# Optimization experiments

Hardware: AMD Instinct MI355X
Metric: run time of the kernel (lower is better)

## Reference

```python
import jax, jax.numpy as jnp
import numpy as np

N_NODES = 50000
N_EDGES = 400000
D = 512
LN_EPS = 1e-5


def setup_inputs() -> dict:
    key = jax.random.key(0)
    k0, k1, k2, k3 = jax.random.split(key, 4)
    x = jax.random.normal(k0, (N_NODES, D), dtype=jnp.float32)
    src = jax.random.randint(k1, (N_EDGES,), 0, N_NODES, dtype=jnp.int64)
    dst = jax.random.randint(k2, (N_EDGES,), 0, N_NODES, dtype=jnp.int64)
    W = jax.random.normal(k3, (D, D), dtype=jnp.float32) * 0.05
    b = jnp.zeros((D,), dtype=jnp.float32)
    gamma = jnp.ones((D,), dtype=jnp.float32)
    beta = jnp.zeros((D,), dtype=jnp.float32)
    return {"x": x, "W": W, "b": b, "gamma": gamma, "beta": beta, "src": src, "dst": dst}


def reference(x, W, b, gamma, beta, src, dst):
    n = x.shape[0]
    ones = jnp.ones(src.shape, dtype=x.dtype)
    # DGL GraphConv norm='both': clamp degrees to >= 1
    deg_out = jnp.clip(jax.ops.segment_sum(ones, src, num_segments=n), 1.0)  # [N]
    deg_in = jnp.clip(jax.ops.segment_sum(ones, dst, num_segments=n), 1.0)   # [N]
    h = x * jax.lax.rsqrt(deg_out)[:, None]                 # [N, D] src normalization
    agg = jax.ops.segment_sum(h[src], dst, num_segments=n)  # gather->scatter-add SpMM
    h = agg * jax.lax.rsqrt(deg_in)[:, None]                # dst normalization
    h = h @ W + b                                           # dense linear
    # LayerNorm over last dim
    mu = jnp.mean(h, axis=-1, keepdims=True)
    var = jnp.mean(jnp.square(h - mu), axis=-1, keepdims=True)
    h = (h - mu) * jax.lax.rsqrt(var + LN_EPS) * gamma + beta
    # torch nn.GELU default = exact erf GELU
    return jax.nn.gelu(h, approximate=False)
```

## Files before the change

### kernel.cpp

```cpp
#include <hip/hip_runtime.h>
#include <hip/hip_bf16.h>

#define D 512

typedef __attribute__((ext_vector_type(8))) short bf16x8;
typedef __attribute__((ext_vector_type(4))) float f32x4;

__device__ inline float b2f(short h) {
    union { unsigned u; float f; } c;
    c.u = ((unsigned)(unsigned short)h) << 16;
    return c.f;
}

__global__ void k_hist(const int* __restrict__ src, const int* __restrict__ dst,
                       int* __restrict__ deg_out, int* __restrict__ deg_in, int E) {
    int e = blockIdx.x * 256 + threadIdx.x;
    if (e < E) {
        atomicAdd(&deg_out[src[e]], 1);
        atomicAdd(&deg_in[dst[e]], 1);
    }
}

__global__ __launch_bounds__(256)
void k_scale(const float* __restrict__ x, const int* __restrict__ deg_out,
             __hip_bfloat16* __restrict__ xs, int total16) {
    int i = blockIdx.x * 256 + threadIdx.x;
    if (i >= total16) return;
    int node = i >> 6;
    float w = rsqrtf((float)max(deg_out[node], 1));
    const float4* p = (const float4*)(x + (size_t)i * 8);
    float4 a = p[0], b = p[1];
    union { float4 f4; __hip_bfloat16 h[8]; } o;
    o.h[0] = __float2bfloat16(a.x * w);
    o.h[1] = __float2bfloat16(a.y * w);
    o.h[2] = __float2bfloat16(a.z * w);
    o.h[3] = __float2bfloat16(a.w * w);
    o.h[4] = __float2bfloat16(b.x * w);
    o.h[5] = __float2bfloat16(b.y * w);
    o.h[6] = __float2bfloat16(b.z * w);
    o.h[7] = __float2bfloat16(b.w * w);
    *(float4*)(xs + (size_t)i * 8) = o.f4;
}

__global__ void k_scan1(const int* __restrict__ deg_in, int* __restrict__ row_start,
                        int* __restrict__ partials, int N) {
    __shared__ int sm[1024];
    int tid = threadIdx.x;
    int i = blockIdx.x * 1024 + tid;
    int v = (i < N) ? deg_in[i] : 0;
    sm[tid] = v;
    __syncthreads();
    int acc = v;
    #pragma unroll
    for (int off = 1; off < 1024; off <<= 1) {
        int t = (tid >= off) ? sm[tid - off] : 0;
        __syncthreads();
        acc += t;
        sm[tid] = acc;
        __syncthreads();
    }
    if (i < N) row_start[i] = acc - v;
    if (tid == 1023) partials[blockIdx.x] = acc;
}

__global__ void k_scan2w(int* __restrict__ partials, int* __restrict__ row_start,
                         int nb, int N) {
    int lane = threadIdx.x;
    int orig = (lane < nb) ? partials[lane] : 0;
    int v = orig;
    #pragma unroll
    for (int off = 1; off < 64; off <<= 1) {
        int t = __shfl_up(v, off, 64);
        if (lane >= off) v += t;
    }
    if (lane < nb) partials[lane] = v - orig;
    if (lane == 63) row_start[N] = v;
}

__global__ void k_scan2s(int* __restrict__ partials, int* __restrict__ row_start,
                         int nb, int N) {
    if (threadIdx.x == 0 && blockIdx.x == 0) {
        int run = 0;
        for (int b = 0; b < nb; b++) { int t = partials[b]; partials[b] = run; run += t; }
        row_start[N] = run;
    }
}

__global__ void k_scan3(int* __restrict__ row_start, const int* __restrict__ partials, int N) {
    int i = blockIdx.x * 256 + threadIdx.x;
    if (i < N) row_start[i] += partials[i >> 10];
}

__global__ void k_fill(const int* __restrict__ src, const int* __restrict__ dst,
                       const int* __restrict__ row_start, int* __restrict__ cursor,
                       int* __restrict__ csr_src, int E) {
    int e = blockIdx.x * 256 + threadIdx.x;
    if (e < E) {
        int d = dst[e];
        int slot = atomicAdd(&cursor[d], 1);
        csr_src[row_start[d] + slot] = src[e];
    }
}

__global__ __launch_bounds__(1024)
void k_spmm(const __hip_bfloat16* __restrict__ xs, const int* __restrict__ row_start,
            const int* __restrict__ csr_src, __hip_bfloat16* __restrict__ Ap, int N) {
    int wid = threadIdx.x >> 6;
    int lane = threadIdx.x & 63;
    int node = blockIdx.x * 16 + wid;
    if (node >= N) return;
    int rs = row_start[node], re = row_start[node + 1];

    float acc[8];
    #pragma unroll
    for (int k = 0; k < 8; k++) acc[k] = 0.f;
    const __hip_bfloat16* xl = xs + (size_t)lane * 8;

    int j = rs;
    for (; j + 4 <= re; j += 4) {
        int s0 = csr_src[j], s1 = csr_src[j + 1], s2 = csr_src[j + 2], s3 = csr_src[j + 3];
        bf16x8 v0 = *(const bf16x8*)(xl + (size_t)s0 * D);
        bf16x8 v1 = *(const bf16x8*)(xl + (size_t)s1 * D);
        bf16x8 v2 = *(const bf16x8*)(xl + (size_t)s2 * D);
        bf16x8 v3 = *(const bf16x8*)(xl + (size_t)s3 * D);
        #pragma unroll
        for (int k = 0; k < 8; k++)
            acc[k] += (b2f(v0[k]) + b2f(v1[k])) + (b2f(v2[k]) + b2f(v3[k]));
    }
    for (; j < re; j++) {
        int s = csr_src[j];
        bf16x8 v = *(const bf16x8*)(xl + (size_t)s * D);
        #pragma unroll
        for (int k = 0; k < 8; k++) acc[k] += b2f(v[k]);
    }

    float rn = rsqrtf((float)max(re - rs, 1));
    union { float4 f4; __hip_bfloat16 h[8]; } o;
    #pragma unroll
    for (int k = 0; k < 8; k++) o.h[k] = __float2bfloat16(acc[k] * rn);
    *(float4*)((char*)Ap + ((size_t)(node >> 4) * 1024 + lane * 16 + (node & 15)) * 16) = o.f4;
}

__global__ __launch_bounds__(256)
void k_spmm_f32(const float* __restrict__ x, const int* __restrict__ row_start,
                const int* __restrict__ csr_src, const int* __restrict__ deg_out,
                __hip_bfloat16* __restrict__ A, int N) {
    int wid = threadIdx.x >> 6;
    int lane = threadIdx.x & 63;
    int node = blockIdx.x * 4 + wid;
    if (node >= N) return;
    int rs = row_start[node], re = row_start[node + 1];
    float4 acc0 = {0.f, 0.f, 0.f, 0.f};
    float4 acc1 = {0.f, 0.f, 0.f, 0.f};
    const float* xl = x + (size_t)lane * 8;
    for (int j = rs; j < re; j++) {
        int s = csr_src[j];
        float w = rsqrtf((float)max(deg_out[s], 1));
        const float4* p = (const float4*)(xl + (size_t)s * D);
        float4 a = p[0], b = p[1];
        acc0.x += a.x * w; acc0.y += a.y * w; acc0.z += a.z * w; acc0.w += a.w * w;
        acc1.x += b.x * w; acc1.y += b.y * w; acc1.z += b.z * w; acc1.w += b.w * w;
    }
    float rn = rsqrtf((float)max(re - rs, 1));
    union { float4 f4; __hip_bfloat16 h[8]; } o;
    o.h[0] = __float2bfloat16(acc0.x * rn);
    o.h[1] = __float2bfloat16(acc0.y * rn);
    o.h[2] = __float2bfloat16(acc0.z * rn);
    o.h[3] = __float2bfloat16(acc0.w * rn);
    o.h[4] = __float2bfloat16(acc1.x * rn);
    o.h[5] = __float2bfloat16(acc1.y * rn);
    o.h[6] = __float2bfloat16(acc1.z * rn);
    o.h[7] = __float2bfloat16(acc1.w * rn);
    *(float4*)(A + (size_t)node * D + lane * 8) = o.f4;
}

__global__ void k_packw2(const float* __restrict__ W, __hip_bfloat16* __restrict__ Wp) {
    int bid = blockIdx.x;
    int c = bid >> 7, kt = (bid >> 3) & 15, ntc = bid & 7;
    int lane = threadIdx.x;
    int k0 = kt * 32 + (lane >> 4) * 8;
    int n  = (c * 8 + ntc) * 16 + (lane & 15);
    union { float4 f4; __hip_bfloat16 h[8]; } o;
    #pragma unroll
    for (int j = 0; j < 8; j++)
        o.h[j] = __float2bfloat16(W[(size_t)(k0 + j) * D + n]);
    *(float4*)(Wp + ((size_t)bid * 64 + lane) * 8) = o.f4;
}

__global__ void k_packw(const float* __restrict__ W, __hip_bfloat16* __restrict__ Wp) {
    int tile = blockIdx.x;
    int lane = threadIdx.x;
    int kt = tile >> 5, nt = tile & 31;
    int k0 = kt * 32 + (lane >> 4) * 8;
    int n  = nt * 16 + (lane & 15);
    union { float4 f4; __hip_bfloat16 h[8]; } o;
    #pragma unroll
    for (int j = 0; j < 8; j++)
        o.h[j] = __float2bfloat16(W[(size_t)(k0 + j) * D + n]);
    *(float4*)(Wp + ((size_t)tile * 64 + lane) * 8) = o.f4;
}

__global__ __launch_bounds__(512, 4)
void k_gemm3(const __hip_bfloat16* __restrict__ Ap, const __hip_bfloat16* __restrict__ Wp,
             const float* __restrict__ bias, const float* __restrict__ gamma,
             const float* __restrict__ beta, float* __restrict__ out, int M) {
    __shared__ float s_sum[64][4];
    __shared__ float s_sq[64][4];

    int tid = threadIdx.x;
    int wid = tid >> 6, lane = tid & 63;
    int wm = wid >> 2, wn = wid & 3;
    int l4 = lane >> 4, coll = lane & 15;
    int tb = blockIdx.x * 64;
    int rgmax = ((M + 15) >> 4) - 1;

    int rg0 = (tb >> 4) + wm * 2;
    int rgA = min(rg0, rgmax);
    int rgB = min(rg0 + 1, rgmax);
    const char* a0 = (const char*)Ap + (size_t)rgA * 16384 + (size_t)lane * 16;
    const char* a1 = (const char*)Ap + (size_t)rgB * 16384 + (size_t)lane * 16;
    const char* wb = (const char*)Wp + ((size_t)(wn * 128) * 64 + lane) * 16;

    f32x4 acc0[8], acc1[8];
    #pragma unroll
    for (int t = 0; t < 8; t++) { acc0[t] = (f32x4){0,0,0,0}; acc1[t] = (f32x4){0,0,0,0}; }

    for (int kt = 0; kt < 16; kt++) {
        bf16x8 af0 = *(const bf16x8*)(a0 + (size_t)kt * 1024);
        bf16x8 af1 = *(const bf16x8*)(a1 + (size_t)kt * 1024);
        const char* wk = wb + (size_t)kt * 8192;
        #pragma unroll
        for (int t = 0; t < 8; t++) {
            bf16x8 bf = *(const bf16x8*)(wk + (size_t)t * 1024);
            acc0[t] = __builtin_amdgcn_mfma_f32_16x16x32_bf16(af0, bf, acc0[t], 0, 0, 0);
            acc1[t] = __builtin_amdgcn_mfma_f32_16x16x32_bf16(af1, bf, acc1[t], 0, 0, 0);
        }
    }

    float bia[8], gam[8], bet[8];
    #pragma unroll
    for (int t = 0; t < 8; t++) {
        int col = wn * 128 + t * 16 + coll;
        bia[t] = bias[col]; gam[t] = gamma[col]; bet[t] = beta[col];
    }
    #pragma unroll
    for (int ai = 0; ai < 2; ai++) {
        f32x4* acc = ai ? acc1 : acc0;
        #pragma unroll
        for (int r = 0; r < 4; r++) {
            float s = 0.f, q = 0.f;
            #pragma unroll
            for (int t = 0; t < 8; t++) {
                float v = acc[t][r] + bia[t];
                acc[t][r] = v;
                s += v; q += v * v;
            }
            #pragma unroll
            for (int off = 1; off < 16; off <<= 1) {
                s += __shfl_xor(s, off, 64);
                q += __shfl_xor(q, off, 64);
            }
            if (coll == 0) {
                int rb = wm * 32 + ai * 16 + l4 * 4 + r;
                s_sum[rb][wn] = s;
                s_sq[rb][wn] = q;
            }
        }
    }
    __syncthreads();

    #pragma unroll
    for (int ai = 0; ai < 2; ai++) {
        f32x4* acc = ai ? acc1 : acc0;
        #pragma unroll
        for (int r = 0; r < 4; r++) {
            int rb = wm * 32 + ai * 16 + l4 * 4 + r;
            int gr = tb + rb;
            if (gr >= M) continue;
            float s = s_sum[rb][0] + s_sum[rb][1] + s_sum[rb][2] + s_sum[rb][3];
            float q = s_sq[rb][0] + s_sq[rb][1] + s_sq[rb][2] + s_sq[rb][3];
            float mean = s * (1.0f / 512.0f);
            float var = q * (1.0f / 512.0f) - mean * mean;
            float rstd = rsqrtf(fmaxf(var, 0.f) + 1e-5f);
            float* orow = out + (size_t)gr * D + wn * 128 + coll;
            #pragma unroll
            for (int t = 0; t < 8; t++) {
                float y = (acc[t][r] - mean) * rstd * gam[t] + bet[t];
                float yy = y * y;
                float pz = fmaf(yy, -0.1029423374f, -2.3022076728f);
                float e = __builtin_amdgcn_exp2f(y * pz);
                float g = y * __builtin_amdgcn_rcpf(1.0f + e);
                orow[t * 16] = g;
            }
        }
    }
}

__global__ __launch_bounds__(512)
void k_gemm(const __hip_bfloat16* __restrict__ A, const __hip_bfloat16* __restrict__ Wp,
            const float* __restrict__ bias, const float* __restrict__ gamma,
            const float* __restrict__ beta, float* __restrict__ out, int M) {
    int tid = threadIdx.x;
    int wid = tid >> 6, lane = tid & 63;
    int wm = wid >> 2;
    int wn = wid & 3;
    int l4 = lane >> 4, coll = lane & 15;
    int m0 = blockIdx.x * 32 + wm * 16;
    int arow = m0 + coll;
    bool rowok = (arow < M);

    f32x4 acc[8];
    #pragma unroll
    for (int t = 0; t < 8; t++) acc[t] = (f32x4){0.f, 0.f, 0.f, 0.f};

    const bf16x8* wpb = (const bf16x8*)Wp;
    for (int kt = 0; kt < 16; kt++) {
        bf16x8 afrag;
        if (rowok) afrag = *(const bf16x8*)(A + (size_t)arow * D + kt * 32 + l4 * 8);
        else afrag = (bf16x8){0,0,0,0,0,0,0,0};
        const bf16x8* wp = wpb + ((size_t)(kt * 32 + wn * 8) * 64 + lane);
        #pragma unroll
        for (int t = 0; t < 8; t++) {
            bf16x8 bfrag = wp[(size_t)t * 64];
            acc[t] = __builtin_amdgcn_mfma_f32_16x16x32_bf16(afrag, bfrag, acc[t], 0, 0, 0);
        }
    }
    __shared__ float s_sum[32][4];
    __shared__ float s_sq[32][4];
    #pragma unroll
    for (int r = 0; r < 4; r++) {
        float s = 0.f, q = 0.f;
        #pragma unroll
        for (int t = 0; t < 8; t++) {
            int col = wn * 128 + t * 16 + coll;
            float v = acc[t][r] + bias[col];
            acc[t][r] = v;
            s += v; q += v * v;
        }
        #pragma unroll
        for (int off = 1; off < 16; off <<= 1) {
            s += __shfl_xor(s, off, 64);
            q += __shfl_xor(q, off, 64);
        }
        if (coll == 0) {
            int rb = wm * 16 + l4 * 4 + r;
            s_sum[rb][wn] = s;
            s_sq[rb][wn] = q;
        }
    }
    __syncthreads();
    #pragma unroll
    for (int r = 0; r < 4; r++) {
        int rb = wm * 16 + l4 * 4 + r;
        int gr = blockIdx.x * 32 + rb;
        if (gr >= M) continue;
        float s = s_sum[rb][0] + s_sum[rb][1] + s_sum[rb][2] + s_sum[rb][3];
        float q = s_sq[rb][0] + s_sq[rb][1] + s_sq[rb][2] + s_sq[rb][3];
        float mean = s * (1.0f / 512.0f);
        float var = q * (1.0f / 512.0f) - mean * mean;
        float rstd = rsqrtf(fmaxf(var, 0.f) + 1e-5f);
        #pragma unroll
        for (int t = 0; t < 8; t++) {
            int col = wn * 128 + t * 16 + coll;
            float y = (acc[t][r] - mean) * rstd * gamma[col] + beta[col];
            float yy = y * y;
            float pz = fmaf(yy, -0.1029423374f, -2.3022076728f);
            float e = __builtin_amdgcn_exp2f(y * pz);
            out[(size_t)gr * D + col] = y * __builtin_amdgcn_rcpf(1.0f + e);
        }
    }
}

extern "C" void kernel_launch(void* const* d_in, const int* in_sizes, int n_in,
                              void* d_out, int out_size, void* d_ws, size_t ws_size,
                              hipStream_t stream) {
    const float* x     = (const float*)d_in[0];
    const float* W     = (const float*)d_in[1];
    const float* b     = (const float*)d_in[2];
    const float* gamma = (const float*)d_in[3];
    const float* beta  = (const float*)d_in[4];
    const int*   src   = (const int*)d_in[5];
    const int*   dst   = (const int*)d_in[6];
    int N = in_sizes[0] / D;
    int E = in_sizes[5];
    float* out = (float*)d_out;

    int* deg_out   = (int*)d_ws;
    int* deg_in    = deg_out + N;
    int* row_start = deg_in + N;
    int* cursor    = row_start + N + 1;
    int* partials  = cursor + N;
    int* csr_src   = partials + 64;
    uintptr_t p = (uintptr_t)(csr_src + E);
    p = (p + 255) & ~(uintptr_t)255;
    __hip_bfloat16* A = (__hip_bfloat16*)p;
    p += (size_t)(((N + 15) / 16) * 16) * D * sizeof(__hip_bfloat16);
    p = (p + 255) & ~(uintptr_t)255;
    __hip_bfloat16* Wp = (__hip_bfloat16*)p;
    p += (size_t)D * D * sizeof(__hip_bfloat16);
    p = (p + 255) & ~(uintptr_t)255;
    __hip_bfloat16* xs = (__hip_bfloat16*)p;
    size_t need_xs = (p - (uintptr_t)d_ws) + (size_t)N * D * sizeof(__hip_bfloat16);
    bool use_bf16_path = (ws_size >= need_xs);

    hipMemsetAsync(deg_out, 0, (size_t)2 * N * sizeof(int), stream);
    hipMemsetAsync(cursor, 0, (size_t)N * sizeof(int), stream);

    k_hist<<<(E + 255) / 256, 256, 0, stream>>>(src, dst, deg_out, deg_in, E);
    int nb1 = (N + 1023) / 1024;
    k_scan1<<<nb1, 1024, 0, stream>>>(deg_in, row_start, partials, N);
    if (nb1 <= 64)
        k_scan2w<<<1, 64, 0, stream>>>(partials, row_start, nb1, N);
    else
        k_scan2s<<<1, 64, 0, stream>>>(partials, row_start, nb1, N);
    k_scan3<<<(N + 255) / 256, 256, 0, stream>>>(row_start, partials, N);
    k_fill<<<(E + 255) / 256, 256, 0, stream>>>(src, dst, row_start, cursor, csr_src, E);

    if (use_bf16_path) {
        int total16 = N * 64;
        k_scale<<<(total16 + 255) / 256, 256, 0, stream>>>(x, deg_out, xs, total16);
        k_spmm<<<(N + 15) / 16, 1024, 0, stream>>>(xs, row_start, csr_src, A, N);
        k_packw2<<<512, 64, 0, stream>>>(W, Wp);
        k_gemm3<<<(N + 63) / 64, 512, 0, stream>>>(A, Wp, b, gamma, beta, out, N);
    } else {
        k_spmm_f32<<<(N + 3) / 4, 256, 0, stream>>>(x, row_start, csr_src, deg_out, A, N);
        k_packw<<<512, 64, 0, stream>>>(W, Wp);
        k_gemm<<<(N + 31) / 32, 512, 0, stream>>>(A, Wp, b, gamma, beta, out, N);
    }
}
```

Before: 240.6 us.

## Use row-major A for GEMM, seed cursor in scan, drop memset, smaller SpMM blocks

The SpMM output A moves from a fragment-packed tiled layout back to plain row-major. The GEMM kernel now loads 16-byte A fragments per row directly, and its output stores become nontemporal. The CSR fill cursor is initialised to the row start inside the scan kernel, which removes one memset and one row_start load per edge. SpMM blocks shrink from 1024 to 256 threads. The row-major A loads are less coalesced than the packed layout, which trades GEMM load efficiency for simpler SpMM stores.

```diff
diff --git a/kernel.cpp b/kernel.cpp
--- a/kernel.cpp
+++ b/kernel.cpp
@@ -86,28 +86,31 @@
     }
 }
 
-__global__ void k_scan3(int* __restrict__ row_start, const int* __restrict__ partials, int N) {
+__global__ void k_scan3(int* __restrict__ row_start, int* __restrict__ cursor,
+                        const int* __restrict__ partials, int N) {
     int i = blockIdx.x * 256 + threadIdx.x;
-    if (i < N) row_start[i] += partials[i >> 10];
+    if (i < N) {
+        int v = row_start[i] + partials[i >> 10];
+        row_start[i] = v;
+        cursor[i] = v;
+    }
 }
 
 __global__ void k_fill(const int* __restrict__ src, const int* __restrict__ dst,
-                       const int* __restrict__ row_start, int* __restrict__ cursor,
-                       int* __restrict__ csr_src, int E) {
+                       int* __restrict__ cursor, int* __restrict__ csr_src, int E) {
     int e = blockIdx.x * 256 + threadIdx.x;
     if (e < E) {
-        int d = dst[e];
-        int slot = atomicAdd(&cursor[d], 1);
-        csr_src[row_start[d] + slot] = src[e];
-    }
-}
-
-__global__ __launch_bounds__(1024)
+        int slot = atomicAdd(&cursor[dst[e]], 1);
+        csr_src[slot] = src[e];
+    }
+}
+
+__global__ __launch_bounds__(256)
 void k_spmm(const __hip_bfloat16* __restrict__ xs, const int* __restrict__ row_start,
-            const int* __restrict__ csr_src, __hip_bfloat16* __restrict__ Ap, int N) {
+            const int* __restrict__ csr_src, __hip_bfloat16* __restrict__ A, int N) {
     int wid = threadIdx.x >> 6;
     int lane = threadIdx.x & 63;
-    int node = blockIdx.x * 16 + wid;
+    int node = blockIdx.x * 4 + wid;
     if (node >= N) return;
     int rs = row_start[node], re = row_start[node + 1];
 
@@ -138,7 +141,116 @@
     union { float4 f4; __hip_bfloat16 h[8]; } o;
     #pragma unroll
     for (int k = 0; k < 8; k++) o.h[k] = __float2bfloat16(acc[k] * rn);
-    *(float4*)((char*)Ap + ((size_t)(node >> 4) * 1024 + lane * 16 + (node & 15)) * 16) = o.f4;
+    *(float4*)(A + (size_t)node * D + lane * 8) = o.f4;
+}
+
+__global__ void k_packw2(const float* __restrict__ W, __hip_bfloat16* __restrict__ Wp) {
+    int bid = blockIdx.x;
+    int c = bid >> 7, kt = (bid >> 3) & 15, ntc = bid & 7;
+    int lane = threadIdx.x;
+    int k0 = kt * 32 + (lane >> 4) * 8;
+    int n  = (c * 8 + ntc) * 16 + (lane & 15);
+    union { float4 f4; __hip_bfloat16 h[8]; } o;
+    #pragma unroll
+    for (int j = 0; j < 8; j++)
+        o.h[j] = __float2bfloat16(W[(size_t)(k0 + j) * D + n]);
+    *(float4*)(Wp + ((size_t)bid * 64 + lane) * 8) = o.f4;
+}
+
+__global__ __launch_bounds__(512, 4)
+void k_gemm3r(const __hip_bfloat16* __restrict__ A, const __hip_bfloat16* __restrict__ Wp,
+              const float* __restrict__ bias, const float* __restrict__ gamma,
+              const float* __restrict__ beta, float* __restrict__ out, int M) {
+    __shared__ float s_sum[64][4];
+    __shared__ float s_sq[64][4];
+
+    int tid = threadIdx.x;
+    int wid = tid >> 6, lane = tid & 63;
+    int wm = wid >> 2, wn = wid & 3;
+    int l4 = lane >> 4, coll = lane & 15;
+    int tb = blockIdx.x * 64;
+
+    int r0 = wm * 32 + coll;
+    int r1 = r0 + 16;
+    int gA = min(tb + r0, M - 1);
+    int gB = min(tb + r1, M - 1);
+    const char* a0 = (const char*)A + (size_t)gA * 1024 + l4 * 16;
+    const char* a1 = (const char*)A + (size_t)gB * 1024 + l4 * 16;
+    const char* wb = (const char*)Wp + ((size_t)(wn * 128) * 64 + lane) * 16;
+
+    f32x4 acc0[8], acc1[8];
+    #pragma unroll
+    for (int t = 0; t < 8; t++) { acc0[t] = (f32x4){0,0,0,0}; acc1[t] = (f32x4){0,0,0,0}; }
+
+    for (int kt = 0; kt < 16; kt++) {
+        bf16x8 af0 = *(const bf16x8*)(a0 + (size_t)kt * 64);
+        bf16x8 af1 = *(const bf16x8*)(a1 + (size_t)kt * 64);
+        const char* wk = wb + (size_t)kt * 8192;
+        #pragma unroll
+        for (int t = 0; t < 8; t++) {
+            bf16x8 bf = *(const bf16x8*)(wk + (size_t)t * 1024);
+            acc0[t] = __builtin_amdgcn_mfma_f32_16x16x32_bf16(af0, bf, acc0[t], 0, 0, 0);
+            acc1[t] = __builtin_amdgcn_mfma_f32_16x16x32_bf16(af1, bf, acc1[t], 0, 0, 0);
+        }
+    }
+
+    float bia[8], gam[8], bet[8];
+    #pragma unroll
+    for (int t = 0; t < 8; t++) {
+        int col = wn * 128 + t * 16 + coll;
+        bia[t] = bias[col]; gam[t] = gamma[col]; bet[t] = beta[col];
+    }
+    #pragma unroll
+    for (int ai = 0; ai < 2; ai++) {
+        f32x4* acc = ai ? acc1 : acc0;
+        #pragma unroll
+        for (int r = 0; r < 4; r++) {
+            float s = 0.f, q = 0.f;
+            #pragma unroll
+            for (int t = 0; t < 8; t++) {
+                float v = acc[t][r] + bia[t];
+                acc[t][r] = v;
+                s += v; q += v * v;
+            }
+            #pragma unroll
+            for (int off = 1; off < 16; off <<= 1) {
+                s += __shfl_xor(s, off, 64);
+                q += __shfl_xor(q, off, 64);
+            }
+            if (coll == 0) {
+                int rb = wm * 32 + ai * 16 + l4 * 4 + r;
+                s_sum[rb][wn] = s;
+                s_sq[rb][wn] = q;
+            }
+        }
+    }
+    __syncthreads();
+
+    #pragma unroll
+    for (int ai = 0; ai < 2; ai++) {
+        f32x4* acc = ai ? acc1 : acc0;
+        #pragma unroll
+        for (int r = 0; r < 4; r++) {
+            int rb = wm * 32 + ai * 16 + l4 * 4 + r;
+            int gr = tb + rb;
+            if (gr >= M) continue;
+            float s = s_sum[rb][0] + s_sum[rb][1] + s_sum[rb][2] + s_sum[rb][3];
+            float q = s_sq[rb][0] + s_sq[rb][1] + s_sq[rb][2] + s_sq[rb][3];
+            float mean = s * (1.0f / 512.0f);
+            float var = q * (1.0f / 512.0f) - mean * mean;
+            float rstd = rsqrtf(fmaxf(var, 0.f) + 1e-5f);
+            float* orow = out + (size_t)gr * D + wn * 128 + coll;
+            #pragma unroll
+            for (int t = 0; t < 8; t++) {
+                float y = (acc[t][r] - mean) * rstd * gam[t] + bet[t];
+                float yy = y * y;
+                float pz = fmaf(yy, -0.1029423374f, -2.3022076728f);
+                float e = __builtin_amdgcn_exp2f(y * pz);
+                float g = y * __builtin_amdgcn_rcpf(1.0f + e);
+                __builtin_nontemporal_store(g, orow + t * 16);
+            }
+        }
+    }
 }
 
 __global__ __launch_bounds__(256)
@@ -174,19 +286,6 @@
     *(float4*)(A + (size_t)node * D + lane * 8) = o.f4;
 }
 
-__global__ void k_packw2(const float* __restrict__ W, __hip_bfloat16* __restrict__ Wp) {
-    int bid = blockIdx.x;
-    int c = bid >> 7, kt = (bid >> 3) & 15, ntc = bid & 7;
-    int lane = threadIdx.x;
-    int k0 = kt * 32 + (lane >> 4) * 8;
-    int n  = (c * 8 + ntc) * 16 + (lane & 15);
-    union { float4 f4; __hip_bfloat16 h[8]; } o;
-    #pragma unroll
-    for (int j = 0; j < 8; j++)
-        o.h[j] = __float2bfloat16(W[(size_t)(k0 + j) * D + n]);
-    *(float4*)(Wp + ((size_t)bid * 64 + lane) * 8) = o.f4;
-}
-
 __global__ void k_packw(const float* __restrict__ W, __hip_bfloat16* __restrict__ Wp) {
     int tile = blockIdx.x;
     int lane = threadIdx.x;
@@ -198,102 +297,6 @@
     for (int j = 0; j < 8; j++)
         o.h[j] = __float2bfloat16(W[(size_t)(k0 + j) * D + n]);
     *(float4*)(Wp + ((size_t)tile * 64 + lane) * 8) = o.f4;
-}
-
-__global__ __launch_bounds__(512, 4)
-void k_gemm3(const __hip_bfloat16* __restrict__ Ap, const __hip_bfloat16* __restrict__ Wp,
-             const float* __restrict__ bias, const float* __restrict__ gamma,
-             const float* __restrict__ beta, float* __restrict__ out, int M) {
-    __shared__ float s_sum[64][4];
-    __shared__ float s_sq[64][4];
-
-    int tid = threadIdx.x;
-    int wid = tid >> 6, lane = tid & 63;
-    int wm = wid >> 2, wn = wid & 3;
-    int l4 = lane >> 4, coll = lane & 15;
-    int tb = blockIdx.x * 64;
-    int rgmax = ((M + 15) >> 4) - 1;
-
-    int rg0 = (tb >> 4) + wm * 2;
-    int rgA = min(rg0, rgmax);
-    int rgB = min(rg0 + 1, rgmax);
-    const char* a0 = (const char*)Ap + (size_t)rgA * 16384 + (size_t)lane * 16;
-    const char* a1 = (const char*)Ap + (size_t)rgB * 16384 + (size_t)lane * 16;
-    const char* wb = (const char*)Wp + ((size_t)(wn * 128) * 64 + lane) * 16;
-
-    f32x4 acc0[8], acc1[8];
-    #pragma unroll
-    for (int t = 0; t < 8; t++) { acc0[t] = (f32x4){0,0,0,0}; acc1[t] = (f32x4){0,0,0,0}; }
-
-    for (int kt = 0; kt < 16; kt++) {
-        bf16x8 af0 = *(const bf16x8*)(a0 + (size_t)kt * 1024);
-        bf16x8 af1 = *(const bf16x8*)(a1 + (size_t)kt * 1024);
-        const char* wk = wb + (size_t)kt * 8192;
-        #pragma unroll
-        for (int t = 0; t < 8; t++) {
-            bf16x8 bf = *(const bf16x8*)(wk + (size_t)t * 1024);
-            acc0[t] = __builtin_amdgcn_mfma_f32_16x16x32_bf16(af0, bf, acc0[t], 0, 0, 0);
-            acc1[t] = __builtin_amdgcn_mfma_f32_16x16x32_bf16(af1, bf, acc1[t], 0, 0, 0);
-        }
-    }
-
-    float bia[8], gam[8], bet[8];
-    #pragma unroll
-    for (int t = 0; t < 8; t++) {
-        int col = wn * 128 + t * 16 + coll;
-        bia[t] = bias[col]; gam[t] = gamma[col]; bet[t] = beta[col];
-    }
-    #pragma unroll
-    for (int ai = 0; ai < 2; ai++) {
-        f32x4* acc = ai ? acc1 : acc0;
-        #pragma unroll
-        for (int r = 0; r < 4; r++) {
-            float s = 0.f, q = 0.f;
-            #pragma unroll
-            for (int t = 0; t < 8; t++) {
-                float v = acc[t][r] + bia[t];
-                acc[t][r] = v;
-                s += v; q += v * v;
-            }
-            #pragma unroll
-            for (int off = 1; off < 16; off <<= 1) {
-                s += __shfl_xor(s, off, 64);
-                q += __shfl_xor(q, off, 64);
-            }
-            if (coll == 0) {
-                int rb = wm * 32 + ai * 16 + l4 * 4 + r;
-                s_sum[rb][wn] = s;
-                s_sq[rb][wn] = q;
-            }
-        }
-    }
-    __syncthreads();
-
-    #pragma unroll
-    for (int ai = 0; ai < 2; ai++) {
-        f32x4* acc = ai ? acc1 : acc0;
-        #pragma unroll
-        for (int r = 0; r < 4; r++) {
-            int rb = wm * 32 + ai * 16 + l4 * 4 + r;
-            int gr = tb + rb;
-            if (gr >= M) continue;
-            float s = s_sum[rb][0] + s_sum[rb][1] + s_sum[rb][2] + s_sum[rb][3];
-            float q = s_sq[rb][0] + s_sq[rb][1] + s_sq[rb][2] + s_sq[rb][3];
-            float mean = s * (1.0f / 512.0f);
-            float var = q * (1.0f / 512.0f) - mean * mean;
-            float rstd = rsqrtf(fmaxf(var, 0.f) + 1e-5f);
-            float* orow = out + (size_t)gr * D + wn * 128 + coll;
-            #pragma unroll
-            for (int t = 0; t < 8; t++) {
-                float y = (acc[t][r] - mean) * rstd * gam[t] + bet[t];
-                float yy = y * y;
-                float pz = fmaf(yy, -0.1029423374f, -2.3022076728f);
-                float e = __builtin_amdgcn_exp2f(y * pz);
-                float g = y * __builtin_amdgcn_rcpf(1.0f + e);
-                orow[t * 16] = g;
-            }
-        }
-    }
 }
 
 __global__ __launch_bounds__(512)
@@ -394,17 +397,16 @@
     uintptr_t p = (uintptr_t)(csr_src + E);
     p = (p + 255) & ~(uintptr_t)255;
     __hip_bfloat16* A = (__hip_bfloat16*)p;
-    p += (size_t)(((N + 15) / 16) * 16) * D * sizeof(__hip_bfloat16);
+    p += (size_t)N * D * sizeof(__hip_bfloat16);
     p = (p + 255) & ~(uintptr_t)255;
     __hip_bfloat16* Wp = (__hip_bfloat16*)p;
     p += (size_t)D * D * sizeof(__hip_bfloat16);
     p = (p + 255) & ~(uintptr_t)255;
     __hip_bfloat16* xs = (__hip_bfloat16*)p;
     size_t need_xs = (p - (uintptr_t)d_ws) + (size_t)N * D * sizeof(__hip_bfloat16);
-    bool use_bf16_path = (ws_size >= need_xs);
+    bool main_path = (ws_size >= need_xs);
 
     hipMemsetAsync(deg_out, 0, (size_t)2 * N * sizeof(int), stream);
-    hipMemsetAsync(cursor, 0, (size_t)N * sizeof(int), stream);
 
     k_hist<<<(E + 255) / 256, 256, 0, stream>>>(src, dst, deg_out, deg_in, E);
     int nb1 = (N + 1023) / 1024;
@@ -413,15 +415,15 @@
         k_scan2w<<<1, 64, 0, stream>>>(partials, row_start, nb1, N);
     else
         k_scan2s<<<1, 64, 0, stream>>>(partials, row_start, nb1, N);
-    k_scan3<<<(N + 255) / 256, 256, 0, stream>>>(row_start, partials, N);
-    k_fill<<<(E + 255) / 256, 256, 0, stream>>>(src, dst, row_start, cursor, csr_src, E);
-
-    if (use_bf16_path) {
+    k_scan3<<<(N + 255) / 256, 256, 0, stream>>>(row_start, cursor, partials, N);
+    k_fill<<<(E + 255) / 256, 256, 0, stream>>>(src, dst, cursor, csr_src, E);
+
+    if (main_path) {
         int total16 = N * 64;
         k_scale<<<(total16 + 255) / 256, 256, 0, stream>>>(x, deg_out, xs, total16);
-        k_spmm<<<(N + 15) / 16, 1024, 0, stream>>>(xs, row_start, csr_src, A, N);
+        k_spmm<<<(N + 3) / 4, 256, 0, stream>>>(xs, row_start, csr_src, A, N);
         k_packw2<<<512, 64, 0, stream>>>(W, Wp);
-        k_gemm3<<<(N + 63) / 64, 512, 0, stream>>>(A, Wp, b, gamma, beta, out, N);
+        k_gemm3r<<<(N + 63) / 64, 512, 0, stream>>>(A, Wp, b, gamma, beta, out, N);
     } else {
         k_spmm_f32<<<(N + 3) / 4, 256, 0, stream>>>(x, row_start, csr_src, deg_out, A, N);
         k_packw<<<512, 64, 0, stream>>>(W, Wp);
```

After: 245.5 us. 2.1% more time.
